# Kernel optimization log

Hardware: AMD Instinct MI355X
Metric: run time of the kernel (lower is better)

The kernel has to match this reference:

```python
import jax, jax.numpy as jnp
import numpy as np

B, S, D_MODEL = 2, 2048, 1024
N_HEADS, D_HEAD = 16, 64
ATTN_SCALE = float(np.sqrt(D_HEAD))
IGNORE = -100000.0


def setup_inputs() -> dict:
    key = jax.random.key(0)
    ks = jax.random.split(key, 8)
    scale = 1.0 / np.sqrt(D_MODEL)
    return {
        "x": jax.random.normal(ks[0], (B, S, D_MODEL), jnp.float32),
        "pos_embed": jax.random.normal(ks[1], (B, S, D_MODEL), jnp.float32),
        "W_Q": jax.random.normal(ks[2], (N_HEADS, D_MODEL, D_HEAD), jnp.float32) * scale,
        "b_Q": jnp.zeros((N_HEADS, D_HEAD), jnp.float32),
        "W_K": jax.random.normal(ks[3], (N_HEADS, D_MODEL, D_HEAD), jnp.float32) * scale,
        "b_K": jnp.zeros((N_HEADS, D_HEAD), jnp.float32),
        "W_V": jax.random.normal(ks[4], (N_HEADS, D_MODEL, D_HEAD), jnp.float32) * scale,
        "b_V": jnp.zeros((N_HEADS, D_HEAD), jnp.float32),
        "W_O": jax.random.normal(ks[5], (N_HEADS, D_HEAD, D_MODEL), jnp.float32) * (1.0 / np.sqrt(D_HEAD)),
        "b_O": jnp.zeros((D_MODEL,), jnp.float32),
    }


def reference(x, pos_embed, W_Q, b_Q, W_K, b_K, W_V, b_V, W_O, b_O):
    # use_pos_resid=False: q,k read x+pos_embed, v reads x
    attn_input = x + pos_embed                                   # [b,p,m]
    q = jnp.einsum('bpm,imh->bpih', attn_input, W_Q) + b_Q       # [b,p,i,h]
    k = jnp.einsum('bpm,imh->bpih', attn_input, W_K) + b_K
    v = jnp.einsum('bpm,imh->bpih', x, W_V) + b_V
    # scores[b,i,p,q]: query index p attends to key index q
    scores = jnp.einsum('bpih,bqih->bipq', q, k) / ATTN_SCALE
    S_len = scores.shape[-1]
    causal = jnp.tril(jnp.ones((S_len, S_len), bool))
    scores = jnp.where(causal, scores, IGNORE)
    attn = jax.nn.softmax(scores, axis=-1)                       # [b,i,q_dst,p_src]
    z = jnp.einsum('bpih,biqp->bqih', v, attn)                   # [b,q,i,h]
    out = jnp.einsum('bqih,ihm->bqm', z, W_O) + b_O              # [b,q,m]
    return out
```

## Files before the change

### kernel.cpp

```cpp
#include <hip/hip_runtime.h>
#include <hip/hip_bf16.h>
#include <stdint.h>

typedef __hip_bfloat16 bf16;
typedef __attribute__((ext_vector_type(8))) short short8;
typedef __attribute__((ext_vector_type(4))) short short4v;
typedef __attribute__((ext_vector_type(4))) float f32x4;
typedef __attribute__((ext_vector_type(16))) float f32x16;
typedef __attribute__((ext_vector_type(4))) unsigned uint4v;
typedef __attribute__((ext_vector_type(2))) unsigned uint2v;

#define AS1 __attribute__((address_space(1)))
#define AS3 __attribute__((address_space(3)))

static constexpr int SEQ = 2048, DM = 1024, DHD = 64;
static constexpr int MROWS = 2 * SEQ;

__device__ __forceinline__ short f2b(float f) {
  __hip_bfloat16 h = __float2bfloat16(f);
  return *reinterpret_cast<short*>(&h);
}

__device__ __forceinline__ unsigned pack2(float lo, float hi) {
  float2 fv; fv.x = lo; fv.y = hi;
  union { __hip_bfloat162 h; unsigned u; } cv;
  cv.h = __float22bfloat162_rn(fv);
  return cv.u;
}

union U8 { uint4v u; short8 s; };

#define GL16(dst, ptr, off) \
  asm volatile("global_load_dwordx4 %0, %1, off offset:" #off : "=v"(dst) : "v"(ptr))
#define WAITV(n) do { asm volatile("s_waitcnt vmcnt(" #n ")"); __builtin_amdgcn_sched_barrier(0); } while (0)

__device__ __forceinline__ float xmax32(float v) {
#if __has_builtin(__builtin_amdgcn_permlane32_swap)
  uint2v r = __builtin_amdgcn_permlane32_swap(__float_as_uint(v), __float_as_uint(v), false, false);
  return fmaxf(__uint_as_float(r[0]), __uint_as_float(r[1]));
#else
  return fmaxf(v, __shfl_xor(v, 32));
#endif
}
__device__ __forceinline__ float xsum32(float v) {
#if __has_builtin(__builtin_amdgcn_permlane32_swap)
  uint2v r = __builtin_amdgcn_permlane32_swap(__float_as_uint(v), __float_as_uint(v), false, false);
  return __uint_as_float(r[0]) + __uint_as_float(r[1]);
#else
  return v + __shfl_xor(v, 32);
#endif
}

__global__ __launch_bounds__(256) void prep_inputs(const float* __restrict__ x,
                                                   const float* __restrict__ pos,
                                                   bf16* __restrict__ xb,
                                                   bf16* __restrict__ aib) {
  int i = blockIdx.x * 256 + threadIdx.x;
  const int n4 = MROWS * DM / 4;
  if (i >= n4) return;
  f32x4 xv = ((const f32x4*)x)[i];
  f32x4 pv = ((const f32x4*)pos)[i];
  short4v xo, ao;
#pragma unroll
  for (int j = 0; j < 4; ++j) {
    xo[j] = f2b(xv[j]);
    ao[j] = f2b(xv[j] + pv[j]);
  }
  ((short4v*)xb)[i] = xo;
  ((short4v*)aib)[i] = ao;
}

__global__ __launch_bounds__(256) void transpose_w(const float* __restrict__ in,
                                                   bf16* __restrict__ out, int R, int C) {
  __shared__ float t[64][65];
  int ct = blockIdx.x, rt = blockIdx.y, z = blockIdx.z;
  in += (size_t)z * R * C;
  out += (size_t)z * R * C;
  int c = threadIdx.x & 63, g = threadIdx.x >> 6;
#pragma unroll
  for (int j = 0; j < 16; ++j) {
    int r = g * 16 + j;
    t[r][c] = in[(size_t)(rt * 64 + r) * C + (ct * 64 + c)];
  }
  __syncthreads();
#pragma unroll
  for (int j = 0; j < 16; ++j) {
    int rr = g * 16 + j;
    out[(size_t)(ct * 64 + rr) * R + (rt * 64 + c)] = __float2bfloat16(t[c][rr]);
  }
}

template <int MODE, typename OutT>
__device__ __forceinline__ void gemm128_body(const bf16* __restrict__ A,
                                             const bf16* __restrict__ Bt,
                                             const float* __restrict__ bias,
                                             OutT* __restrict__ C, int mt, int nt,
                                             float scale) {
  __shared__ alignas(16) bf16 Al[128 * 32];
  __shared__ alignas(16) bf16 Bl[128 * 32];
  const int lane = threadIdx.x & 63, wv = threadIdx.x >> 6;
  const int wr = wv >> 1, wc = wv & 1;
  const bf16* Ab = A + (size_t)mt * 128 * DM;
  const bf16* Bb = Bt + (size_t)nt * 128 * DM;

  f32x4 acc[4][4];
#pragma unroll
  for (int i = 0; i < 4; ++i)
#pragma unroll
    for (int j = 0; j < 4; ++j) acc[i][j] = (f32x4){0.f, 0.f, 0.f, 0.f};

  for (int kt = 0; kt < DM / 32; ++kt) {
    int k0 = kt * 32;
#pragma unroll
    for (int c = 0; c < 2; ++c) {
      int li0 = wv * 64 + c * 256;
      int li = li0 + lane;
      int row = li >> 2, sl = li & 3;
      int gs = sl ^ ((row >> 1) & 3);
      __builtin_amdgcn_global_load_lds((const AS1 void*)(Ab + (size_t)row * DM + k0 + gs * 8),
                                       (AS3 void*)(&Al[li0 * 8]), 16, 0, 0);
    }
#pragma unroll
    for (int c = 0; c < 2; ++c) {
      int li0 = wv * 64 + c * 256;
      int li = li0 + lane;
      int row = li >> 2, sl = li & 3;
      int gs = sl ^ ((row >> 1) & 3);
      __builtin_amdgcn_global_load_lds((const AS1 void*)(Bb + (size_t)row * DM + k0 + gs * 8),
                                       (AS3 void*)(&Bl[li0 * 8]), 16, 0, 0);
    }
    __syncthreads();

    short8 af[4], bfr[4];
    const int kb = lane >> 4;
#pragma unroll
    for (int mi = 0; mi < 4; ++mi) {
      int r = wr * 64 + mi * 16 + (lane & 15);
      af[mi] = *(const short8*)(&Al[r * 32 + ((kb ^ ((r >> 1) & 3)) << 3)]);
    }
#pragma unroll
    for (int ni = 0; ni < 4; ++ni) {
      int r = wc * 64 + ni * 16 + (lane & 15);
      bfr[ni] = *(const short8*)(&Bl[r * 32 + ((kb ^ ((r >> 1) & 3)) << 3)]);
    }
#pragma unroll
    for (int mi = 0; mi < 4; ++mi)
#pragma unroll
      for (int ni = 0; ni < 4; ++ni)
        acc[mi][ni] = __builtin_amdgcn_mfma_f32_16x16x32_bf16(af[mi], bfr[ni], acc[mi][ni], 0, 0, 0);
    __syncthreads();
  }

#pragma unroll
  for (int mi = 0; mi < 4; ++mi) {
#pragma unroll
    for (int ni = 0; ni < 4; ++ni) {
      int row0 = mt * 128 + wr * 64 + mi * 16 + (lane >> 4) * 4;
      int col = nt * 128 + wc * 64 + ni * 16 + (lane & 15);
      float bv = bias[col];
      if constexpr (MODE == 1) {
#pragma unroll
        for (int j = 0; j < 4; ++j)
          C[(size_t)(row0 + j) * DM + col] = (acc[mi][ni][j] + bv) * scale;
      } else {
        int bb = row0 >> 11, s0 = row0 & 2047;
        int hh = col >> 6, d0 = col & 63;
        size_t bhb = (size_t)(bb * 16 + hh) * 131072;
        if constexpr (MODE == 3) {
          int kc = d0 >> 4, hi = (d0 >> 3) & 1, e = d0 & 7;
          int g = s0 >> 5, r0 = s0 & 31;
          size_t bbase = bhb + g * 2048 + kc * 512 + e;
#pragma unroll
          for (int j = 0; j < 4; ++j)
            ((bf16*)C)[bbase + (size_t)(r0 + j + 32 * hi) * 8] =
                __float2bfloat16((acc[mi][ni][j] + bv) * scale);
        } else {
          int dj = d0 >> 5, d32 = d0 & 31;
          int ks = s0 >> 4, hi2 = (s0 >> 3) & 1, e0 = s0 & 7;
          short4v o;
#pragma unroll
          for (int j = 0; j < 4; ++j) o[j] = f2b(acc[mi][ni][j] + bv);
          *(short4v*)((bf16*)C + bhb + dj * 65536 + ks * 512 + (size_t)(d32 + 32 * hi2) * 8 + e0) = o;
        }
      }
    }
  }
}

static constexpr float QSCALE = 0.125f * 1.4426950408889634f;

__global__ __launch_bounds__(256) void qkv_gemm(const bf16* __restrict__ aib,
                                                const bf16* __restrict__ xb,
                                                const bf16* __restrict__ wqt,
                                                const bf16* __restrict__ wkt,
                                                const bf16* __restrict__ wvt,
                                                const float* __restrict__ bq,
                                                const float* __restrict__ bk,
                                                const float* __restrict__ bv,
                                                bf16* __restrict__ FQ, bf16* __restrict__ FK,
                                                bf16* __restrict__ FV) {
  int mt = blockIdx.x & 31;
  int nt = (blockIdx.x >> 5) & 7;
  int mat = blockIdx.x >> 8;
  if (mat == 0) {
    gemm128_body<3>(aib, wqt, bq, FQ, mt, nt, QSCALE);
  } else if (mat == 1) {
    gemm128_body<3>(aib, wkt, bk, FK, mt, nt, 1.0f);
  } else {
    gemm128_body<4>(xb, wvt, bv, FV, mt, nt, 1.0f);
  }
}

__global__ __launch_bounds__(256) void o_gemm(const bf16* __restrict__ Z,
                                              const bf16* __restrict__ wot,
                                              const float* __restrict__ bo,
                                              float* __restrict__ out) {
  int mt = blockIdx.x & 31;
  int nt = blockIdx.x >> 5;
  gemm128_body<1>(Z, wot, bo, out, mt, nt, 1.0f);
}

__global__ __launch_bounds__(128, 2) void flash_attn(const bf16* __restrict__ FQ,
                                                     const bf16* __restrict__ FK,
                                                     const bf16* __restrict__ FV,
                                                     bf16* __restrict__ Zb) {
  __shared__ float Zm[64][33];
  __shared__ float Ml[64], Ll[64];
  __shared__ unsigned Zl[32 * 32];

  const int lane = threadIdx.x & 63;
  const int wvi = threadIdx.x >> 6;
  const int qln = lane & 31;
  const bool hib = lane >= 32;
  const int bh = blockIdx.x & 31;
  const int wq = 63 - (blockIdx.x >> 5);
  const int bb = bh >> 4, h = bh & 15;
  const int q0 = wq * 32;
  const int nt = wq / 2 + 1;
  const int hsp = (nt + 1) >> 1;
  const int t0 = wvi ? hsp : 0;
  const int t1 = wvi ? nt : hsp;

  const size_t fb = (size_t)bh * 131072;
  const bf16* qp = FQ + fb + wq * 2048 + lane * 8;
  const bf16* kpt = FK + fb + (size_t)t0 * 4096 + lane * 8;
  const bf16* vp0 = FV + fb + (size_t)t0 * 2048 + lane * 8;
  const bf16* vp1 = vp0 + 65536;

  f32x16 zacc[2];
#pragma unroll
  for (int i = 0; i < 16; ++i) { zacc[0][i] = 0.f; zacc[1][i] = 0.f; }
  float mrun = -1e30f, lrun = 0.f;

  short8 qf[4];
  short8 kfA[2][4], kfB[2][4];

  if (t0 < t1) {
    GL16(qf[0], qp, 0); GL16(qf[1], qp, 1024); GL16(qf[2], qp, 2048); GL16(qf[3], qp, 3072);
    {
      const bf16* k1 = kpt + 2048;
      GL16(kfA[0][0], kpt, 0); GL16(kfA[0][1], kpt, 1024); GL16(kfA[0][2], kpt, 2048); GL16(kfA[0][3], kpt, 3072);
      GL16(kfA[1][0], k1, 0);  GL16(kfA[1][1], k1, 1024);  GL16(kfA[1][2], k1, 2048);  GL16(kfA[1][3], k1, 3072);
      kpt += 4096;
    }

    auto computeT = [&](short8(&kf)[2][4], short8(&kfn)[2][4], int t) {
      const int kv0 = t * 64;
      const bool pref = (t + 1 < t1);

      short8 vf[2][4];
      GL16(vf[0][0], vp0, 0); GL16(vf[0][1], vp0, 1024); GL16(vf[0][2], vp0, 2048); GL16(vf[0][3], vp0, 3072);
      GL16(vf[1][0], vp1, 0); GL16(vf[1][1], vp1, 1024); GL16(vf[1][2], vp1, 2048); GL16(vf[1][3], vp1, 3072);
      vp0 += 2048; vp1 += 2048;

      WAITV(8);

      f32x16 s[2];
#pragma unroll
      for (int i = 0; i < 16; ++i) { s[0][i] = 0.f; s[1][i] = 0.f; }
#pragma unroll
      for (int kc = 0; kc < 4; ++kc) {
        s[0] = __builtin_amdgcn_mfma_f32_32x32x16_bf16(kf[0][kc], qf[kc], s[0], 0, 0, 0);
        s[1] = __builtin_amdgcn_mfma_f32_32x32x16_bf16(kf[1][kc], qf[kc], s[1], 0, 0, 0);
      }

      if (pref) {
        const bf16* k1 = kpt + 2048;
        GL16(kfn[0][0], kpt, 0); GL16(kfn[0][1], kpt, 1024); GL16(kfn[0][2], kpt, 2048); GL16(kfn[0][3], kpt, 3072);
        GL16(kfn[1][0], k1, 0);  GL16(kfn[1][1], k1, 1024);  GL16(kfn[1][2], k1, 2048);  GL16(kfn[1][3], k1, 3072);
        kpt += 4096;
      }

      if (t == nt - 1) {
        const int qg = q0 + qln;
#pragma unroll
        for (int ni = 0; ni < 2; ++ni)
#pragma unroll
          for (int rr = 0; rr < 16; ++rr) {
            int kv = kv0 + 32 * ni + (rr & 3) + 8 * (rr >> 2) + (hib ? 4 : 0);
            if (kv > qg) s[ni][rr] = -1e30f;
          }
      }

      float t8[8];
#pragma unroll
      for (int i = 0; i < 8; ++i)
        t8[i] = fmaxf(fmaxf(s[0][i], s[0][i + 8]), fmaxf(s[1][i], s[1][i + 8]));
      float tm = fmaxf(fmaxf(fmaxf(t8[0], t8[1]), fmaxf(t8[2], t8[3])),
                       fmaxf(fmaxf(t8[4], t8[5]), fmaxf(t8[6], t8[7])));
      tm = xmax32(tm);

      if (__ballot(tm > mrun)) {
        float mn = fmaxf(mrun, tm);
        float al = exp2f(mrun - mn);
        mrun = mn;
        lrun *= al;
#pragma unroll
        for (int i = 0; i < 16; ++i) { zacc[0][i] *= al; zacc[1][i] *= al; }
      }

      float pacc[4] = {0.f, 0.f, 0.f, 0.f};
#pragma unroll
      for (int ni = 0; ni < 2; ++ni)
#pragma unroll
        for (int rr = 0; rr < 16; ++rr) {
          float p = exp2f(s[ni][rr] - mrun);
          s[ni][rr] = p;
          pacc[rr & 3] += p;
        }
      lrun += xsum32((pacc[0] + pacc[1]) + (pacc[2] + pacc[3]));

      unsigned su32[2][8];
#pragma unroll
      for (int ni = 0; ni < 2; ++ni)
#pragma unroll
        for (int tt = 0; tt < 8; ++tt)
          su32[ni][tt] = pack2(s[ni][2 * tt], s[ni][2 * tt + 1]);

      short8 pa[4];
#if __has_builtin(__builtin_amdgcn_permlane32_swap)
#pragma unroll
      for (int c = 0; c < 4; ++c) {
        int ni = c >> 1, b4 = 4 * (c & 1);
        uint2v r0 = __builtin_amdgcn_permlane32_swap(su32[ni][b4 + 0], su32[ni][b4 + 2], false, false);
        uint2v r1 = __builtin_amdgcn_permlane32_swap(su32[ni][b4 + 1], su32[ni][b4 + 3], false, false);
        U8 w;
        w.u[0] = r0[0]; w.u[1] = r1[0]; w.u[2] = r0[1]; w.u[3] = r1[1];
        pa[c] = w.s;
      }
#else
      unsigned X[2][8];
#pragma unroll
      for (int ni = 0; ni < 2; ++ni)
#pragma unroll
        for (int tt = 0; tt < 8; ++tt)
          X[ni][tt] = (unsigned)__shfl_xor((int)su32[ni][tt], 32);
#pragma unroll
      for (int c = 0; c < 4; ++c) {
        int ni = c >> 1, b4 = 4 * (c & 1);
        U8 w;
        w.u[0] = hib ? X[ni][b4 + 2] : su32[ni][b4 + 0];
        w.u[1] = hib ? X[ni][b4 + 3] : su32[ni][b4 + 1];
        w.u[2] = hib ? su32[ni][b4 + 2] : X[ni][b4 + 0];
        w.u[3] = hib ? su32[ni][b4 + 3] : X[ni][b4 + 1];
        pa[c] = w.s;
      }
#endif

      if (pref) { WAITV(8); } else { WAITV(0); }

#pragma unroll
      for (int c = 0; c < 4; ++c) {
        zacc[0] = __builtin_amdgcn_mfma_f32_32x32x16_bf16(vf[0][c], pa[c], zacc[0], 0, 0, 0);
        zacc[1] = __builtin_amdgcn_mfma_f32_32x32x16_bf16(vf[1][c], pa[c], zacc[1], 0, 0, 0);
      }
    };

    int t = t0;
    while (true) {
      computeT(kfA, kfB, t);
      if (++t >= t1) break;
      computeT(kfB, kfA, t);
      if (++t >= t1) break;
    }
  }

  if (wvi == 1) {
#pragma unroll
    for (int i = 0; i < 16; ++i) {
      Zm[lane][i] = zacc[0][i];
      Zm[lane][16 + i] = zacc[1][i];
    }
    Ml[lane] = mrun;
    Ll[lane] = lrun;
  }
  __syncthreads();
  if (wvi == 0) {
    float m1 = Ml[lane], l1 = Ll[lane];
    float mn = fmaxf(mrun, m1);
    float a0 = exp2f(mrun - mn);
    float a1 = exp2f(m1 - mn);
    float lm = lrun * a0 + l1 * a1;
#pragma unroll
    for (int i = 0; i < 16; ++i) {
      zacc[0][i] = zacc[0][i] * a0 + Zm[lane][i] * a1;
      zacc[1][i] = zacc[1][i] * a0 + Zm[lane][16 + i] * a1;
    }

    const float rl = 1.0f / lm;
    const int W8[8] = {0, 1, 4, 5, 8, 9, 12, 13};
#pragma unroll
    for (int dj = 0; dj < 2; ++dj)
#pragma unroll
      for (int tt = 0; tt < 8; ++tt) {
        unsigned v = pack2(zacc[dj][2 * tt] * rl, zacc[dj][2 * tt + 1] * rl);
        int x = 16 * dj + (hib ? 2 : 0) + W8[tt];
        Zl[qln * 32 + (((x >> 2) ^ (qln & 7)) << 2) + (x & 3)] = v;
      }
    asm volatile("s_waitcnt lgkmcnt(0)" ::: "memory");
    __builtin_amdgcn_sched_barrier(0);
    const size_t base = ((size_t)bb * SEQ) * DM + h * DHD;
    int q2 = lane >> 1, hf = lane & 1;
#pragma unroll
    for (int u = 0; u < 4; ++u) {
      int sl = (hf * 4 + u) ^ (q2 & 7);
      U8 w;
      w.u = *(const uint4v*)&Zl[q2 * 32 + sl * 4];
      *(short8*)(Zb + base + (size_t)(q0 + q2) * DM + hf * 32 + u * 8) = w.s;
    }
  }
}

extern "C" void kernel_launch(void* const* d_in, const int* in_sizes, int n_in,
                              void* d_out, int out_size, void* d_ws, size_t ws_size,
                              hipStream_t stream) {
  (void)in_sizes; (void)n_in; (void)out_size; (void)ws_size;
  const float* x = (const float*)d_in[0];
  const float* pos = (const float*)d_in[1];
  const float* WQ = (const float*)d_in[2];
  const float* bQ = (const float*)d_in[3];
  const float* WK = (const float*)d_in[4];
  const float* bK = (const float*)d_in[5];
  const float* WV = (const float*)d_in[6];
  const float* bV = (const float*)d_in[7];
  const float* WO = (const float*)d_in[8];
  const float* bO = (const float*)d_in[9];
  float* out = (float*)d_out;

  bf16* ws = (bf16*)d_ws;
  size_t off = 0;
  bf16* aib = ws + off; off += (size_t)MROWS * DM;
  bf16* xb  = ws + off; off += (size_t)MROWS * DM;
  bf16* wqt = ws + off; off += (size_t)DM * DM;
  bf16* wkt = ws + off; off += (size_t)DM * DM;
  bf16* wvt = ws + off; off += (size_t)DM * DM;
  bf16* wot = ws + off; off += (size_t)DM * DM;
  bf16* FQ  = ws + off; off += (size_t)MROWS * DM;
  bf16* FK  = ws + off; off += (size_t)MROWS * DM;
  bf16* FV  = ws + off; off += (size_t)MROWS * DM;
  bf16* Zb  = ws + off; off += (size_t)MROWS * DM;

  prep_inputs<<<(MROWS * DM / 4 + 255) / 256, 256, 0, stream>>>(x, pos, xb, aib);
  dim3 gq(1, 16, 16);
  transpose_w<<<gq, 256, 0, stream>>>(WQ, wqt, 1024, 64);
  transpose_w<<<gq, 256, 0, stream>>>(WK, wkt, 1024, 64);
  transpose_w<<<gq, 256, 0, stream>>>(WV, wvt, 1024, 64);
  dim3 go(16, 16, 1);
  transpose_w<<<go, 256, 0, stream>>>(WO, wot, 1024, 1024);
  qkv_gemm<<<768, 256, 0, stream>>>(aib, xb, wqt, wkt, wvt, bQ, bK, bV, FQ, FK, FV);
  flash_attn<<<2048, 128, 0, stream>>>(FQ, FK, FV, Zb);
  o_gemm<<<256, 256, 0, stream>>>(Zb, wot, bO, out);
}
```

Before: 123.6 us.

## Use 64-row O-projection GEMM tiles, lazy softmax rescale, and native exp2

Replaces the 128x128-tile output-projection GEMM with a 64x128-tile kernel that loads straight into LDS, doubling the block count to 512 so more of the GPU's compute units stay busy. In flash attention, the running max is rescaled only when the new tile max exceeds it by more than 8 (in log2 units), which skips most rescale passes. exp2f is swapped for the hardware exp2 intrinsic. The lazy rescale lets unnormalized exponentials grow up to 2^8, which slightly raises overflow and precision risk for bf16-packed probabilities. The new GEMM is single-buffered and gets less data reuse per block.

```diff
diff --git a/kernel.cpp b/kernel.cpp
--- a/kernel.cpp
+++ b/kernel.cpp
@@ -26,6 +26,14 @@
   union { __hip_bfloat162 h; unsigned u; } cv;
   cv.h = __float22bfloat162_rn(fv);
   return cv.u;
+}
+
+__device__ __forceinline__ float fexp2(float x) {
+#if __has_builtin(__builtin_amdgcn_exp2f)
+  return __builtin_amdgcn_exp2f(x);
+#else
+  return exp2f(x);
+#endif
 }
 
 union U8 { uint4v u; short8 s; };
@@ -211,13 +219,77 @@
   }
 }
 
-__global__ __launch_bounds__(256) void o_gemm(const bf16* __restrict__ Z,
-                                              const bf16* __restrict__ wot,
-                                              const float* __restrict__ bo,
-                                              float* __restrict__ out) {
-  int mt = blockIdx.x & 31;
-  int nt = blockIdx.x >> 5;
-  gemm128_body<1>(Z, wot, bo, out, mt, nt, 1.0f);
+__global__ __launch_bounds__(256) void o_gemm64(const bf16* __restrict__ A,
+                                                const bf16* __restrict__ Bt,
+                                                const float* __restrict__ bias,
+                                                float* __restrict__ out) {
+  __shared__ alignas(16) bf16 Al[64 * 32];
+  __shared__ alignas(16) bf16 Bl[128 * 32];
+  const int mt = blockIdx.x & 63, nt = blockIdx.x >> 6;
+  const int lane = threadIdx.x & 63, wv = threadIdx.x >> 6;
+  const int wr = wv >> 1, wc = wv & 1;
+  const bf16* Ab = A + (size_t)mt * 64 * DM;
+  const bf16* Bb = Bt + (size_t)nt * 128 * DM;
+
+  f32x4 acc[2][4];
+#pragma unroll
+  for (int i = 0; i < 2; ++i)
+#pragma unroll
+    for (int j = 0; j < 4; ++j) acc[i][j] = (f32x4){0.f, 0.f, 0.f, 0.f};
+
+  for (int kt = 0; kt < DM / 32; ++kt) {
+    int k0 = kt * 32;
+    {
+      int li0 = wv * 64;
+      int li = li0 + lane;
+      int row = li >> 2, sl = li & 3;
+      int gs = sl ^ ((row >> 1) & 3);
+      __builtin_amdgcn_global_load_lds((const AS1 void*)(Ab + (size_t)row * DM + k0 + gs * 8),
+                                       (AS3 void*)(&Al[li0 * 8]), 16, 0, 0);
+    }
+#pragma unroll
+    for (int c = 0; c < 2; ++c) {
+      int li0 = wv * 64 + c * 256;
+      int li = li0 + lane;
+      int row = li >> 2, sl = li & 3;
+      int gs = sl ^ ((row >> 1) & 3);
+      __builtin_amdgcn_global_load_lds((const AS1 void*)(Bb + (size_t)row * DM + k0 + gs * 8),
+                                       (AS3 void*)(&Bl[li0 * 8]), 16, 0, 0);
+    }
+    __syncthreads();
+
+    short8 af[2], bfr[4];
+    const int kb = lane >> 4;
+#pragma unroll
+    for (int mi = 0; mi < 2; ++mi) {
+      int r = wr * 32 + mi * 16 + (lane & 15);
+      af[mi] = *(const short8*)(&Al[r * 32 + ((kb ^ ((r >> 1) & 3)) << 3)]);
+    }
+#pragma unroll
+    for (int ni = 0; ni < 4; ++ni) {
+      int r = wc * 64 + ni * 16 + (lane & 15);
+      bfr[ni] = *(const short8*)(&Bl[r * 32 + ((kb ^ ((r >> 1) & 3)) << 3)]);
+    }
+#pragma unroll
+    for (int mi = 0; mi < 2; ++mi)
+#pragma unroll
+      for (int ni = 0; ni < 4; ++ni)
+        acc[mi][ni] = __builtin_amdgcn_mfma_f32_16x16x32_bf16(af[mi], bfr[ni], acc[mi][ni], 0, 0, 0);
+    __syncthreads();
+  }
+
+#pragma unroll
+  for (int mi = 0; mi < 2; ++mi) {
+#pragma unroll
+    for (int ni = 0; ni < 4; ++ni) {
+      int row0 = mt * 64 + wr * 32 + mi * 16 + (lane >> 4) * 4;
+      int col = nt * 128 + wc * 64 + ni * 16 + (lane & 15);
+      float bv = bias[col];
+#pragma unroll
+      for (int j = 0; j < 4; ++j)
+        out[(size_t)(row0 + j) * DM + col] = acc[mi][ni][j] + bv;
+    }
+  }
 }
 
 __global__ __launch_bounds__(128, 2) void flash_attn(const bf16* __restrict__ FQ,
@@ -310,9 +382,9 @@
                        fmaxf(fmaxf(t8[4], t8[5]), fmaxf(t8[6], t8[7])));
       tm = xmax32(tm);
 
-      if (__ballot(tm > mrun)) {
+      if (__ballot(tm > mrun + 8.0f)) {
         float mn = fmaxf(mrun, tm);
-        float al = exp2f(mrun - mn);
+        float al = fexp2(mrun - mn);
         mrun = mn;
         lrun *= al;
 #pragma unroll
@@ -324,7 +396,7 @@
       for (int ni = 0; ni < 2; ++ni)
 #pragma unroll
         for (int rr = 0; rr < 16; ++rr) {
-          float p = exp2f(s[ni][rr] - mrun);
+          float p = fexp2(s[ni][rr] - mrun);
           s[ni][rr] = p;
           pacc[rr & 3] += p;
         }
@@ -398,8 +470,8 @@
   if (wvi == 0) {
     float m1 = Ml[lane], l1 = Ll[lane];
     float mn = fmaxf(mrun, m1);
-    float a0 = exp2f(mrun - mn);
-    float a1 = exp2f(m1 - mn);
+    float a0 = fexp2(mrun - mn);
+    float a1 = fexp2(m1 - mn);
     float lm = lrun * a0 + l1 * a1;
 #pragma unroll
     for (int i = 0; i < 16; ++i) {
@@ -469,5 +541,5 @@
   transpose_w<<<go, 256, 0, stream>>>(WO, wot, 1024, 1024);
   qkv_gemm<<<768, 256, 0, stream>>>(aib, xb, wqt, wkt, wvt, bQ, bK, bV, FQ, FK, FV);
   flash_attn<<<2048, 128, 0, stream>>>(FQ, FK, FV, Zb);
-  o_gemm<<<256, 256, 0, stream>>>(Zb, wot, bO, out);
-}
+  o_gemm64<<<512, 256, 0, stream>>>(Zb, wot, bO, out);
+}
```

New measurement: 113.4 us. -8.3%, faster.
